# Kernel optimization log

Measured on AMD Instinct MI355X. Metric: run time of the kernel, lower is better.

The kernel has to match this reference:

```python
import jax, jax.numpy as jnp
import numpy as np

S, Q, N, T, G = 20000, 32, 200000, 30, 64
D_IN, H, D_SV, D_LANG, D_FUSE = 300, 256, 64, 64, 128

def setup_inputs() -> dict:
    key = jax.random.key(0)
    ks = jax.random.split(key, 20)
    sc = 0.05
    inp = {
        'lang_feat': jax.random.normal(ks[0], (Q, T, D_IN), jnp.float32),
        'supvox_feat': jax.random.normal(ks[1], (S, D_SV), jnp.float32),
        'supvox_coords': jax.random.uniform(ks[2], (S, 3), jnp.float32),
        'lang_len': jax.random.randint(ks[3], (Q,), 5, T + 1).astype(jnp.int32),
        'grps': jax.random.randint(ks[4], (S,), 0, G).astype(jnp.int32),
        'supervox': jax.random.randint(ks[5], (N,), 0, S).astype(jnp.int32),
        'gt': jax.random.randint(ks[6], (N, Q), 0, 2).astype(jnp.int32),
        # GRU params (torch layout: [3H, in])
        'gru_w_ih': sc * jax.random.normal(ks[7], (3 * H, D_IN), jnp.float32),
        'gru_w_hh': sc * jax.random.normal(ks[8], (3 * H, H), jnp.float32),
        'gru_b_ih': sc * jax.random.normal(ks[9], (3 * H,), jnp.float32),
        'gru_b_hh': sc * jax.random.normal(ks[10], (3 * H,), jnp.float32),
        # lang_sqz: Linear(256,64) ReLU Linear(64,64)
        'sqz_w1': sc * jax.random.normal(ks[11], (D_LANG, H), jnp.float32),
        'sqz_b1': sc * jax.random.normal(ks[12], (D_LANG,), jnp.float32),
        'sqz_w2': sc * jax.random.normal(ks[13], (D_LANG, D_LANG), jnp.float32),
        'sqz_b2': sc * jax.random.normal(ks[14], (D_LANG,), jnp.float32),
        # feat_fuse: Linear(131,128) ReLU
        'fuse_w': sc * jax.random.normal(ks[15], (D_FUSE, D_SV + 3 + D_LANG), jnp.float32),
        'fuse_b': sc * jax.random.normal(ks[16], (D_FUSE,), jnp.float32),
        # heat_map: Linear(128,2) (Dropout = identity in eval)
        'heat_w': sc * jax.random.normal(ks[17], (2, D_FUSE), jnp.float32),
        'heat_b': sc * jax.random.normal(ks[18], (2,), jnp.float32),
    }
    return inp

def _gru_last(x, lens, w_ih, w_hh, b_ih, b_hh):
    # x: [Q, T, D_IN]; returns hidden at step lens[q]-1 (pack_padded_sequence semantics)
    def step(h, xt_t):
        xt, t = xt_t  # xt: [Q, D_IN]
        gi = xt @ w_ih.T + b_ih          # [Q, 3H]
        gh = h @ w_hh.T + b_hh           # [Q, 3H]
        ir, iz, inn = jnp.split(gi, 3, -1)
        hr, hz, hn = jnp.split(gh, 3, -1)
        r = jax.nn.sigmoid(ir + hr)
        z = jax.nn.sigmoid(iz + hz)
        n = jnp.tanh(inn + r * hn)
        h_new = (1.0 - z) * n + z * h
        h = jnp.where((t < lens)[:, None], h_new, h)
        return h, None
    h0 = jnp.zeros((x.shape[0], w_hh.shape[1]), x.dtype)
    hT, _ = jax.lax.scan(step, h0, (jnp.swapaxes(x, 0, 1), jnp.arange(x.shape[1])))
    return hT  # [Q, H]

def reference(lang_feat, supvox_feat, supvox_coords, lang_len, grps, supervox, gt,
              gru_w_ih, gru_w_hh, gru_b_ih, gru_b_hh,
              sqz_w1, sqz_b1, sqz_w2, sqz_b2, fuse_w, fuse_b, heat_w, heat_b):
    # language branch
    h = _gru_last(lang_feat, lang_len, gru_w_ih, gru_w_hh, gru_b_ih, gru_b_hh)  # [Q,H]
    lang = jax.nn.relu(h @ sqz_w1.T + sqz_b1) @ sqz_w2.T + sqz_b2               # [Q,64]
    # supervoxel branch: cat(feat, coords) -> [S,67]
    sv = jnp.concatenate([supvox_feat, supvox_coords], -1)
    # feat_fuse on cat(sv, lang): split the weight to avoid materializing [S,Q,131]
    d_sv = sv.shape[-1]
    sv_proj = sv @ fuse_w[:, :d_sv].T           # [S,128]
    lang_proj = lang @ fuse_w[:, d_sv:].T       # [Q,128]
    fused = jax.nn.relu(sv_proj[:, None, :] + lang_proj[None, :, :] + fuse_b)  # [S,Q,128]
    logits = fused @ heat_w.T + heat_b          # [S,Q,2]
    obj_score = jax.nn.softmax(logits, -1)[..., 1]  # [S,Q]
    # cluster-grouped mean score (grps_ one-hot; assumes unique(grps)==arange(G))
    grp_oh = (grps[:, None] == jnp.arange(G)).astype(obj_score.dtype)  # [S,G]
    grp_sum = jnp.einsum('sq,sg->qg', obj_score, grp_oh)               # [Q,G]
    sen_grp_score = grp_sum / grp_oh.sum(0)[None, :]                   # [Q,G]
    best = jnp.argmax(sen_grp_score, -1)        # [Q]
    supvox_sen = grp_oh[:, best]                # [S,Q] binary
    obj_pts = supvox_sen[supervox].astype(jnp.int32)  # [N,Q]
    inter = (obj_pts * gt).sum(0).astype(jnp.float32)
    union = jnp.bitwise_or(obj_pts, gt).sum(0).astype(jnp.float32)
    ious = inter / (union + 1e-5)               # [Q]
    return obj_pts, ious
```

## Files before the change

### kernel.cpp

```cpp
#include <hip/hip_runtime.h>
#include <hip/hip_bf16.h>
#include <math.h>

#define S_TOT 20000
#define Q_TOT 32
#define N_TOT 200000
#define T_MAX 30
#define G_TOT 64
#define D_IN 300
#define H_DIM 256
#define D_SV 64
#define D_LANG 64
#define D_FUSE 128
#define D_CAT 67
#define FW_LD 131
#define SCHUNK 32
#define NBLK3 (S_TOT / SCHUNK)
#define SENT64 0xFFFFFFFFFFFFFFFFull
#define PCHUNK 16
#define PTILES 40

#define GI_MT 32
#define GI_NT 64
#define GI_KC 100
#define GI_NB 12
#define GI_GRID (30 * GI_NB)
#define HG_ELEMS (30 * Q_TOT * H_DIM)

#define SYNCS_N 160

__device__ __forceinline__ float sigmoidf_(float x) { return 1.0f / (1.0f + expf(-x)); }
__device__ __forceinline__ unsigned long long pack2(float a, float b) {
    return ((unsigned long long)__float_as_uint(b) << 32) | (unsigned long long)__float_as_uint(a);
}
__device__ __forceinline__ void tick_wait(int* c, int tgt) {
    __syncthreads();
    if (threadIdx.x == 0) {
        while (__hip_atomic_load(c, __ATOMIC_RELAXED, __HIP_MEMORY_SCOPE_AGENT) < tgt)
            __builtin_amdgcn_s_sleep(4);
    }
    __syncthreads();
}
__device__ __forceinline__ void tick_bump(int* c) {
    asm volatile("s_waitcnt vmcnt(0)" ::: "memory");
    if (threadIdx.x == 0)
        __hip_atomic_fetch_add(c, 1, __ATOMIC_RELAXED, __HIP_MEMORY_SCOPE_AGENT);
}

__global__ __launch_bounds__(128) void k_gi(const float* __restrict__ lang_feat,
                                            const float* __restrict__ w_ih,
                                            const float* __restrict__ b_ih,
                                            const float* __restrict__ fuse_w,
                                            const float* __restrict__ sqz_w1,
                                            const float* __restrict__ sqz_w2,
                                            const float* __restrict__ heat_w,
                                            float* __restrict__ gi,
                                            float* __restrict__ fwt,
                                            float* __restrict__ w1t,
                                            float* __restrict__ w2t,
                                            float* __restrict__ wdr,
                                            float* __restrict__ hg,
                                            int* __restrict__ syncs) {
    const int tid = threadIdx.x;
    if (blockIdx.x >= GI_GRID) {
        const int xb = blockIdx.x - GI_GRID;
        if (xb == 0) {
            for (int i = tid; i < FW_LD * D_FUSE; i += 128)
                fwt[(i % FW_LD) * D_FUSE + (i / FW_LD)] = fuse_w[i];
            for (int i = tid; i < D_LANG * H_DIM; i += 128)
                w1t[(i & 255) * D_LANG + (i >> 8)] = sqz_w1[i];
            for (int i = tid; i < D_LANG * D_LANG; i += 128)
                w2t[(i & 63) * D_LANG + (i >> 6)] = sqz_w2[i];
            if (tid < D_FUSE) wdr[tid] = heat_w[D_FUSE + tid] - heat_w[tid];
        } else {
            const int fb = xb - 1;
            const int per4 = HG_ELEMS / 4 / 8;
            float4* dst = (float4*)hg + fb * per4;
            const float4 sv = make_float4(__uint_as_float(0xFFFFFFFFu), __uint_as_float(0xFFFFFFFFu),
                                          __uint_as_float(0xFFFFFFFFu), __uint_as_float(0xFFFFFFFFu));
            for (int i = tid; i < per4; i += 128) dst[i] = sv;
            if (fb == 0) for (int i = tid; i < SYNCS_N; i += 128) syncs[i] = 0;
        }
        return;
    }
    __shared__ float x_l[GI_KC][GI_MT + 1];
    __shared__ float w_l[GI_KC][GI_NT + 1];
    const int mb = blockIdx.x / GI_NB, nb = blockIdx.x % GI_NB;
    const int m0 = mb * GI_MT, n0 = nb * GI_NT;
    const int tq4 = (tid >> 4) * 4, jq4 = (tid & 15) * 4;

    float acc[4][4];
    #pragma unroll
    for (int i = 0; i < 4; ++i)
        #pragma unroll
        for (int j = 0; j < 4; ++j) acc[i][j] = 0.f;

    for (int kc = 0; kc < 3; ++kc) {
        const int k0 = kc * GI_KC;
        for (int i = tid; i < GI_MT * GI_KC; i += 128) {
            const int r = i / GI_KC, k = i % GI_KC;
            const int row = m0 + r, q = row / T_MAX, t = row - q * T_MAX;
            x_l[k][r] = lang_feat[(q * T_MAX + t) * D_IN + k0 + k];
        }
        for (int i = tid; i < GI_NT * GI_KC; i += 128) {
            const int r = i / GI_KC, k = i % GI_KC;
            w_l[k][r] = w_ih[(n0 + r) * D_IN + k0 + k];
        }
        __syncthreads();
        #pragma unroll 2
        for (int k = 0; k < GI_KC; ++k) {
            const float x0 = x_l[k][tq4 + 0], x1 = x_l[k][tq4 + 1];
            const float x2 = x_l[k][tq4 + 2], x3 = x_l[k][tq4 + 3];
            const float v0 = w_l[k][jq4 + 0], v1 = w_l[k][jq4 + 1];
            const float v2 = w_l[k][jq4 + 2], v3 = w_l[k][jq4 + 3];
            acc[0][0] = fmaf(x0, v0, acc[0][0]); acc[0][1] = fmaf(x0, v1, acc[0][1]);
            acc[0][2] = fmaf(x0, v2, acc[0][2]); acc[0][3] = fmaf(x0, v3, acc[0][3]);
            acc[1][0] = fmaf(x1, v0, acc[1][0]); acc[1][1] = fmaf(x1, v1, acc[1][1]);
            acc[1][2] = fmaf(x1, v2, acc[1][2]); acc[1][3] = fmaf(x1, v3, acc[1][3]);
            acc[2][0] = fmaf(x2, v0, acc[2][0]); acc[2][1] = fmaf(x2, v1, acc[2][1]);
            acc[2][2] = fmaf(x2, v2, acc[2][2]); acc[2][3] = fmaf(x2, v3, acc[2][3]);
            acc[3][0] = fmaf(x3, v0, acc[3][0]); acc[3][1] = fmaf(x3, v1, acc[3][1]);
            acc[3][2] = fmaf(x3, v2, acc[3][2]); acc[3][3] = fmaf(x3, v3, acc[3][3]);
        }
        __syncthreads();
    }
    const float b0 = b_ih[n0 + jq4 + 0], b1 = b_ih[n0 + jq4 + 1];
    const float b2 = b_ih[n0 + jq4 + 2], b3 = b_ih[n0 + jq4 + 3];
    #pragma unroll
    for (int i = 0; i < 4; ++i) {
        const int row = m0 + tq4 + i;
        const int q = row / T_MAX, t = row - q * T_MAX;
        float4 v = make_float4(acc[i][0] + b0, acc[i][1] + b1, acc[i][2] + b2, acc[i][3] + b3);
        *(float4*)&gi[(q * T_MAX + t) * 768 + n0 + jq4] = v;
    }
}

__global__ __launch_bounds__(384, 1) void k_gru8(const float* __restrict__ gi,
                                                 const float* __restrict__ w_hh,
                                                 const float* __restrict__ b_hh,
                                                 const int* __restrict__ lang_len,
                                                 float* __restrict__ hg,
                                                 float* __restrict__ hbuf,
                                                 const float* __restrict__ w1t,
                                                 const float* __restrict__ b1,
                                                 const float* __restrict__ w2t,
                                                 const float* __restrict__ b2,
                                                 const float* __restrict__ fwt,
                                                 const float* __restrict__ fuse_b,
                                                 float* __restrict__ langc,
                                                 int* __restrict__ qdone) {
    __shared__ __align__(16) float wlds[96 * 256];
    __shared__ __align__(16) float hlq[4 * 68];
    __shared__ float ghl[96];
    __shared__ float gil[T_MAX * 96];

    const int tid = threadIdx.x;
    const int q = blockIdx.x >> 3, b = blockIdx.x & 7;
    int len = lang_len[q]; if (len > T_MAX) len = T_MAX; if (len < 1) len = 1;

    {
        const float4* src4 = (const float4*)w_hh;
        float4* dst4 = (float4*)wlds;
        for (int i = tid; i < 96 * 64; i += 384) {
            const int r = i >> 6, c = i & 63;
            const int grow = ((r >> 5) << 8) + (b << 5) + (r & 31);
            dst4[r * 64 + (c ^ (r & 7))] = src4[grow * 64 + c];
        }
    }
    for (int i = tid; i < len * 96; i += 384) {
        const int t = i / 96, r = i % 96;
        gil[i] = gi[(q * T_MAX + t) * 768 + ((r >> 5) << 8) + (b << 5) + (r & 31)];
    }
    __syncthreads();

    float hfin = 0.f;
    {
        float hnew = 0.f;
        if (tid < 32) {
            const float bhr = b_hh[(b << 5) + tid];
            const float bhz = b_hh[H_DIM + (b << 5) + tid];
            const float bhn = b_hh[2 * H_DIM + (b << 5) + tid];
            const float r = sigmoidf_(gil[tid] + bhr);
            const float z = sigmoidf_(gil[32 + tid] + bhz);
            const float n = tanhf(gil[64 + tid] + r * bhn);
            hnew = (1.f - z) * n;
            if (len == 1) hfin = hnew;
        }
        if (tid < 64 && len > 1) {
            const float a0 = __shfl(hnew, 2 * (tid & 15));
            const float a1 = __shfl(hnew, 2 * (tid & 15) + 1);
            if (tid < 16) {
                unsigned long long* dst = (unsigned long long*)(hg + q * H_DIM + (b << 5));
                __hip_atomic_store(dst + tid, pack2(a0, a1), __ATOMIC_RELAXED, __HIP_MEMORY_SCOPE_AGENT);
            }
        }
    }

    const int row = tid >> 2, ql = tid & 3;
    const float bh = b_hh[((row >> 5) << 8) + (b << 5) + (row & 31)];
    const int rx = row & 7;
    const float4* wrow4 = (const float4*)wlds + row * 64;
    const int cbase = ql << 4;

    for (int t = 1; t < len; ++t) {
        if (tid < 128) {
            const unsigned long long* src =
                (const unsigned long long*)(hg + (size_t)(t - 1) * (Q_TOT * H_DIM) + q * H_DIM);
            unsigned long long v;
            while ((v = __hip_atomic_load(src + tid, __ATOMIC_RELAXED,
                                          __HIP_MEMORY_SCOPE_AGENT)) == SENT64)
                __builtin_amdgcn_s_sleep(1);
            const int k = 2 * tid;
            const int o = (k >> 6) * 68 + (k & 63);
            hlq[o]     = __uint_as_float((unsigned)(v & 0xffffffffu));
            hlq[o + 1] = __uint_as_float((unsigned)(v >> 32));
        }
        __syncthreads();
        float hold = 0.f;
        if (tid < 32) { const int k = (b << 5) + tid; hold = hlq[(k >> 6) * 68 + (k & 63)]; }
        const float4* h4 = (const float4*)(hlq + ql * 68);
        float ax = 0.f, ay = 0.f, az = 0.f, aw = 0.f;
        #pragma unroll
        for (int i = 0; i < 16; ++i) {
            const float4 wv = wrow4[(cbase + i) ^ rx];
            const float4 hv = h4[i];
            ax = fmaf(wv.x, hv.x, ax);
            ay = fmaf(wv.y, hv.y, ay);
            az = fmaf(wv.z, hv.z, az);
            aw = fmaf(wv.w, hv.w, aw);
        }
        float s = (ax + ay) + (az + aw);
        s += __shfl_xor(s, 1);
        s += __shfl_xor(s, 2);
        if (ql == 0) ghl[row] = s + bh;
        __syncthreads();
        float hnew = 0.f;
        if (tid < 32) {
            const float* gt_ = gil + t * 96;
            const float r = sigmoidf_(gt_[tid] + ghl[tid]);
            const float z = sigmoidf_(gt_[32 + tid] + ghl[32 + tid]);
            const float n = tanhf(gt_[64 + tid] + r * ghl[64 + tid]);
            hnew = (1.f - z) * n + z * hold;
            if (t == len - 1) hfin = hnew;
        }
        if (tid < 64 && t < len - 1) {
            const float a0 = __shfl(hnew, 2 * (tid & 15));
            const float a1 = __shfl(hnew, 2 * (tid & 15) + 1);
            if (tid < 16) {
                unsigned long long* dst =
                    (unsigned long long*)(hg + (size_t)t * (Q_TOT * H_DIM) + q * H_DIM + (b << 5));
                __hip_atomic_store(dst + tid, pack2(a0, a1), __ATOMIC_RELAXED, __HIP_MEMORY_SCOPE_AGENT);
            }
        }
    }

    if (tid < 32)
        __hip_atomic_store(&hbuf[q * H_DIM + (b << 5) + tid], hfin,
                           __ATOMIC_RELAXED, __HIP_MEMORY_SCOPE_AGENT);
    asm volatile("s_waitcnt vmcnt(0)" ::: "memory");
    __syncthreads();
    if (tid == 0)
        __hip_atomic_fetch_add(&qdone[q], 1, __ATOMIC_RELAXED, __HIP_MEMORY_SCOPE_AGENT);
    if (b != 0) return;

    if (tid == 0) {
        while (__hip_atomic_load(&qdone[q], __ATOMIC_RELAXED, __HIP_MEMORY_SCOPE_AGENT) < 8)
            __builtin_amdgcn_s_sleep(2);
    }
    __syncthreads();
    float* hql = gil;
    float* t1l = gil + 256;
    float* lgl = gil + 320;
    if (tid < H_DIM)
        hql[tid] = __hip_atomic_load(&hbuf[q * H_DIM + tid], __ATOMIC_RELAXED, __HIP_MEMORY_SCOPE_AGENT);
    __syncthreads();
    if (tid < 256) {
        const int c = tid >> 2, qq = tid & 3;
        float a = 0.f;
        #pragma unroll 8
        for (int j = 0; j < 64; ++j) {
            const int k = (qq << 6) + j;
            a = fmaf(w1t[k * D_LANG + c], hql[k], a);
        }
        a += __shfl_xor(a, 1);
        a += __shfl_xor(a, 2);
        if (qq == 0) t1l[c] = fmaxf(a + b1[c], 0.f);
    }
    __syncthreads();
    if (tid < 256) {
        const int c = tid >> 2, qq = tid & 3;
        float a = 0.f;
        #pragma unroll
        for (int j = 0; j < 16; ++j) {
            const int k = (qq << 4) + j;
            a = fmaf(w2t[k * D_LANG + c], t1l[k], a);
        }
        a += __shfl_xor(a, 1);
        a += __shfl_xor(a, 2);
        if (qq == 0) lgl[c] = a + b2[c];
    }
    __syncthreads();
    if (tid < 256) {
        const int d = tid >> 1, hh = tid & 1;
        float a = 0.f;
        #pragma unroll 8
        for (int j = 0; j < 32; ++j) {
            const int k = (hh << 5) + j;
            a = fmaf(fwt[(D_CAT + k) * D_FUSE + d], lgl[k], a);
        }
        a += __shfl_xor(a, 1);
        if (hh == 0) langc[q * D_FUSE + d] = a + fuse_b[d];
    }
}

__global__ __launch_bounds__(256, 3) void k_tail(const float* __restrict__ feat,
                                                 const float* __restrict__ coords,
                                                 const int* __restrict__ grps,
                                                 const float* __restrict__ langc,
                                                 const float* __restrict__ fwt,
                                                 const float* __restrict__ wdr_g,
                                                 const float* __restrict__ heat_b,
                                                 float* __restrict__ grp_part,
                                                 int* __restrict__ cnt_part,
                                                 float* __restrict__ grp2,
                                                 int* __restrict__ cnt2,
                                                 int* __restrict__ best,
                                                 int* __restrict__ smask,
                                                 const int* __restrict__ supervox,
                                                 const int* __restrict__ gt,
                                                 float* __restrict__ out,
                                                 int* __restrict__ syncs) {
    int* interG   = syncs;
    int* unionG   = syncs + 32;
    int* t_out    = syncs + 64;
    int* gtick    = syncs + 65;
    int* qtick    = syncs + 98;
    int* t_fuse   = syncs + 130;
    int* t_smask  = syncs + 131;
    const int tid = threadIdx.x;
    const int bid = blockIdx.x;

    __shared__ __align__(16) float svin[SCHUNK][68];
    __shared__ __align__(16) float svp[SCHUNK][132];
    __shared__ float score[SCHUNK][Q_TOT];
    __shared__ int grps_l[SCHUNK];
    __shared__ float ps[4][G_TOT];
    __shared__ int   pc[4][G_TOT];
    __shared__ float sc[G_TOT];
    __shared__ int bl[Q_TOT];
    __shared__ int bi_s[Q_TOT], bu_s[Q_TOT];
    __shared__ int islast;

    {
        const int s0 = bid * SCHUNK;
        const int dsl = tid & 7, q = tid >> 3;
        float lc[16], wdr[16];
        #pragma unroll
        for (int i = 0; i < 16; ++i) {
            const int d = dsl * 16 + i;
            lc[i]  = langc[q * D_FUSE + d];
            wdr[i] = wdr_g[d];
        }
        const float hbd = heat_b[1] - heat_b[0];

        for (int i = tid; i < SCHUNK * D_SV; i += 256) {
            const int r = i >> 6, c = i & 63;
            svin[r][c] = feat[(s0 + r) * D_SV + c];
        }
        if (tid < SCHUNK * 3) { const int r = tid / 3, c = tid % 3; svin[r][D_SV + c] = coords[(s0 + r) * 3 + c]; }
        if (tid < SCHUNK) grps_l[tid] = grps[s0 + tid];
        __syncthreads();

        {
            const int d = tid & 127, sl0 = tid >> 7;
            float acc[16];
            #pragma unroll
            for (int i = 0; i < 16; ++i) acc[i] = 0.f;
            for (int k4 = 0; k4 < 16; ++k4) {
                const float w0 = fwt[(4 * k4 + 0) * D_FUSE + d];
                const float w1 = fwt[(4 * k4 + 1) * D_FUSE + d];
                const float w2 = fwt[(4 * k4 + 2) * D_FUSE + d];
                const float w3 = fwt[(4 * k4 + 3) * D_FUSE + d];
                #pragma unroll
                for (int i = 0; i < 16; ++i) {
                    const float4 xv = *(const float4*)&svin[sl0 + 2 * i][4 * k4];
                    acc[i] = fmaf(xv.x, w0, fmaf(xv.y, w1, fmaf(xv.z, w2, fmaf(xv.w, w3, acc[i]))));
                }
            }
            for (int k = 64; k < D_CAT; ++k) {
                const float wv = fwt[k * D_FUSE + d];
                #pragma unroll
                for (int i = 0; i < 16; ++i)
                    acc[i] = fmaf(svin[sl0 + 2 * i][k], wv, acc[i]);
            }
            #pragma unroll
            for (int i = 0; i < 16; ++i) svp[sl0 + 2 * i][d] = acc[i];
        }
        __syncthreads();

        for (int sl = 0; sl < SCHUNK; ++sl) {
            const float4* sv4 = (const float4*)(&svp[sl][dsl * 16]);
            float part = 0.f;
            #pragma unroll
            for (int j = 0; j < 4; ++j) {
                const float4 v = sv4[j];
                part = fmaf(fmaxf(v.x + lc[4*j+0], 0.f), wdr[4*j+0], part);
                part = fmaf(fmaxf(v.y + lc[4*j+1], 0.f), wdr[4*j+1], part);
                part = fmaf(fmaxf(v.z + lc[4*j+2], 0.f), wdr[4*j+2], part);
                part = fmaf(fmaxf(v.w + lc[4*j+3], 0.f), wdr[4*j+3], part);
            }
            part += __shfl_xor(part, 1);
            part += __shfl_xor(part, 2);
            part += __shfl_xor(part, 4);
            if (dsl == 0) score[sl][q] = sigmoidf_(part + hbd);
        }
        __syncthreads();

        for (int i = 0; i < 8; ++i) {
            const int cell = tid + 256 * i;
            const int qq = cell >> 6, g = cell & 63;
            float sum = 0.f;
            #pragma unroll
            for (int sl = 0; sl < SCHUNK; ++sl)
                sum += (grps_l[sl] == g) ? score[sl][qq] : 0.f;
            __hip_atomic_store(&grp_part[bid * (Q_TOT * G_TOT) + cell], sum,
                               __ATOMIC_RELAXED, __HIP_MEMORY_SCOPE_AGENT);
            if (cell < G_TOT) {
                int c = 0;
                #pragma unroll
                for (int sl = 0; sl < SCHUNK; ++sl) c += (grps_l[sl] == g);
                __hip_atomic_store(&cnt_part[bid * G_TOT + g], c,
                                   __ATOMIC_RELAXED, __HIP_MEMORY_SCOPE_AGENT);
            }
        }
        tick_bump(t_fuse);
    }
    tick_wait(t_fuse, NBLK3);

    if (bid < Q_TOT * PCHUNK) {
        const int q = bid & 31, c = bid >> 5;
        const int bq = tid >> 6, g = tid & 63;
        const int b0 = c * PTILES;
        int b1 = b0 + PTILES; if (b1 > NBLK3) b1 = NBLK3;
        float acc = 0.f; int cacc = 0;
        for (int b = b0 + bq; b < b1; b += 4) {
            acc  += grp_part[b * (Q_TOT * G_TOT) + q * G_TOT + g];
            cacc += cnt_part[b * G_TOT + g];
        }
        ps[bq][g] = acc; pc[bq][g] = cacc;
        __syncthreads();
        if (tid < G_TOT) {
            const float s = ((ps[0][tid] + ps[1][tid]) + ps[2][tid]) + ps[3][tid];
            const int  cc = ((pc[0][tid] + pc[1][tid]) + pc[2][tid]) + pc[3][tid];
            __hip_atomic_store(&grp2[(c * Q_TOT + q) * G_TOT + tid], s,
                               __ATOMIC_RELAXED, __HIP_MEMORY_SCOPE_AGENT);
            __hip_atomic_store(&cnt2[(c * Q_TOT + q) * G_TOT + tid], cc,
                               __ATOMIC_RELAXED, __HIP_MEMORY_SCOPE_AGENT);
        }
        __shared__ int myturn;
        asm volatile("s_waitcnt vmcnt(0)" ::: "memory");
        if (tid == 0) {
            const int old = __hip_atomic_fetch_add(&qtick[q], 1, __ATOMIC_RELAXED, __HIP_MEMORY_SCOPE_AGENT);
            myturn = (old == PCHUNK - 1) ? 1 : 0;
        }
        __syncthreads();
        if (myturn) {
            if (tid < G_TOT) {
                float s = 0.f; int cc = 0;
                #pragma unroll
                for (int c2 = 0; c2 < PCHUNK; ++c2) {
                    s  += grp2[(c2 * Q_TOT + q) * G_TOT + tid];
                    cc += cnt2[(c2 * Q_TOT + q) * G_TOT + tid];
                }
                sc[tid] = s / (float)cc;
            }
            __syncthreads();
            if (tid == 0) {
                float bv = sc[0]; int bi = 0;
                for (int g2 = 1; g2 < G_TOT; ++g2) if (sc[g2] > bv) { bv = sc[g2]; bi = g2; }
                __hip_atomic_store(&best[q], bi, __ATOMIC_RELAXED, __HIP_MEMORY_SCOPE_AGENT);
                asm volatile("s_waitcnt vmcnt(0)" ::: "memory");
                __hip_atomic_fetch_add(gtick, 1, __ATOMIC_RELAXED, __HIP_MEMORY_SCOPE_AGENT);
            }
        }
    }
    tick_wait(gtick, Q_TOT);

    if (tid < Q_TOT) bl[tid] = best[tid];
    __syncthreads();
    if (tid < 32) {
        const int s = bid * 32 + tid;
        const int gg = grps[s];
        int m = 0;
        #pragma unroll
        for (int qq = 0; qq < Q_TOT; ++qq) m |= (bl[qq] == gg) ? (1 << qq) : 0;
        __hip_atomic_store(&smask[s], m, __ATOMIC_RELAXED, __HIP_MEMORY_SCOPE_AGENT);
    }
    tick_bump(t_smask);
    tick_wait(t_smask, NBLK3);

    {
        const int gidx = bid * 256 + tid;
        const int q4 = (gidx & 7) * 4;
        const int nstride = (NBLK3 * 256) >> 3;
        int a0 = 0, a1 = 0, a2 = 0, a3 = 0;
        int u0 = 0, u1 = 0, u2 = 0, u3 = 0;
        for (int n = gidx >> 3; n < N_TOT; n += nstride) {
            const int m = smask[supervox[n]];
            const int4 g4 = *(const int4*)&gt[n * Q_TOT + q4];
            const int o0 = (m >> (q4 + 0)) & 1;
            const int o1 = (m >> (q4 + 1)) & 1;
            const int o2 = (m >> (q4 + 2)) & 1;
            const int o3 = (m >> (q4 + 3)) & 1;
            *(float4*)&out[n * Q_TOT + q4] =
                make_float4((float)o0, (float)o1, (float)o2, (float)o3);
            a0 += o0 & g4.x; u0 += o0 | g4.x;
            a1 += o1 & g4.y; u1 += o1 | g4.y;
            a2 += o2 & g4.z; u2 += o2 | g4.z;
            a3 += o3 & g4.w; u3 += o3 | g4.w;
        }
        if (tid < Q_TOT) { bi_s[tid] = 0; bu_s[tid] = 0; }
        __syncthreads();
        atomicAdd(&bi_s[q4 + 0], a0); atomicAdd(&bu_s[q4 + 0], u0);
        atomicAdd(&bi_s[q4 + 1], a1); atomicAdd(&bu_s[q4 + 1], u1);
        atomicAdd(&bi_s[q4 + 2], a2); atomicAdd(&bu_s[q4 + 2], u2);
        atomicAdd(&bi_s[q4 + 3], a3); atomicAdd(&bu_s[q4 + 3], u3);
        __syncthreads();
        if (tid < Q_TOT) { atomicAdd(&interG[tid], bi_s[tid]); atomicAdd(&unionG[tid], bu_s[tid]); }
        asm volatile("s_waitcnt vmcnt(0)" ::: "memory");
        if (tid == 0) {
            const int old = __hip_atomic_fetch_add(t_out, 1, __ATOMIC_RELAXED, __HIP_MEMORY_SCOPE_AGENT);
            islast = (old == NBLK3 - 1) ? 1 : 0;
        }
        __syncthreads();
        if (islast && tid < Q_TOT) {
            const int iv = __hip_atomic_load(&interG[tid], __ATOMIC_RELAXED, __HIP_MEMORY_SCOPE_AGENT);
            const int uv = __hip_atomic_load(&unionG[tid], __ATOMIC_RELAXED, __HIP_MEMORY_SCOPE_AGENT);
            out[(size_t)N_TOT * Q_TOT + tid] = (float)iv / ((float)uv + 1e-5f);
        }
    }
}

extern "C" void kernel_launch(void* const* d_in, const int* in_sizes, int n_in,
                              void* d_out, int out_size, void* d_ws, size_t ws_size,
                              hipStream_t stream) {
    const float* lang_feat = (const float*)d_in[0];
    const float* feat      = (const float*)d_in[1];
    const float* coords    = (const float*)d_in[2];
    const int*   lang_len  = (const int*)d_in[3];
    const int*   grps      = (const int*)d_in[4];
    const int*   supervox  = (const int*)d_in[5];
    const int*   gt        = (const int*)d_in[6];
    const float* w_ih      = (const float*)d_in[7];
    const float* w_hh      = (const float*)d_in[8];
    const float* b_ih      = (const float*)d_in[9];
    const float* b_hh      = (const float*)d_in[10];
    const float* sqz_w1    = (const float*)d_in[11];
    const float* sqz_b1    = (const float*)d_in[12];
    const float* sqz_w2    = (const float*)d_in[13];
    const float* sqz_b2    = (const float*)d_in[14];
    const float* fuse_w    = (const float*)d_in[15];
    const float* fuse_b    = (const float*)d_in[16];
    const float* heat_w    = (const float*)d_in[17];
    const float* heat_b    = (const float*)d_in[18];
    float* out = (float*)d_out;

    float* gi       = (float*)d_ws;
    float* hbuf     = gi + 737280;
    float* langc    = hbuf + 8192;
    float* grp_part = langc + 4096;
    int*   cnt_part = (int*)(grp_part + NBLK3 * 2048);
    int*   best     = cnt_part + NBLK3 * 64;
    int*   smask    = best + 32;
    int*   syncs    = smask + S_TOT;
    float* hg       = (float*)(syncs + SYNCS_N);
    float* fwt      = hg + HG_ELEMS;
    float* w1t      = fwt + FW_LD * D_FUSE;
    float* w2t      = w1t + H_DIM * D_LANG;
    float* wdr      = w2t + D_LANG * D_LANG;
    float* grp2     = wdr + 128;
    int*   cnt2     = (int*)(grp2 + PCHUNK * Q_TOT * G_TOT);

    k_gi   <<<GI_GRID + 9, 128, 0, stream>>>(lang_feat, w_ih, b_ih, fuse_w, sqz_w1, sqz_w2, heat_w,
                                             gi, fwt, w1t, w2t, wdr, hg, syncs);
    k_gru8 <<<Q_TOT * 8, 384, 0, stream>>>(gi, w_hh, b_hh, lang_len, hg, hbuf,
                                           w1t, sqz_b1, w2t, sqz_b2, fwt, fuse_b, langc,
                                           syncs + 66);
    k_tail <<<NBLK3, 256, 0, stream>>>(feat, coords, grps, langc, fwt, wdr, heat_b,
                                       grp_part, cnt_part, grp2, cnt2, best, smask,
                                       supervox, gt, out, syncs);
}
```

Before: 234.2 us.

## Replace global grid barriers with per-chunk counters and flag broadcast, drop smask pass

Replaces the all-block barrier after the fuse phase with per-chunk counters, so each partial-reduce block waits only for the PTILES blocks it reads. The group-reduce barrier becomes a set of flags, spread over eight cache lines and written by the last finisher, which cuts contention from polling. The global smask array and its grid-wide barrier go away: each block builds a 64-entry group-to-query mask in shared memory and indexes it through grps[supervox[n]]. The cost is one extra indirect load per point in the output loop. Each block also still spins on a flag.

```diff
diff --git a/kernel.cpp b/kernel.cpp
--- a/kernel.cpp
+++ b/kernel.cpp
@@ -27,24 +27,11 @@
 #define GI_GRID (30 * GI_NB)
 #define HG_ELEMS (30 * Q_TOT * H_DIM)
 
-#define SYNCS_N 160
+#define SYNCS_N 1024
 
 __device__ __forceinline__ float sigmoidf_(float x) { return 1.0f / (1.0f + expf(-x)); }
 __device__ __forceinline__ unsigned long long pack2(float a, float b) {
     return ((unsigned long long)__float_as_uint(b) << 32) | (unsigned long long)__float_as_uint(a);
-}
-__device__ __forceinline__ void tick_wait(int* c, int tgt) {
-    __syncthreads();
-    if (threadIdx.x == 0) {
-        while (__hip_atomic_load(c, __ATOMIC_RELAXED, __HIP_MEMORY_SCOPE_AGENT) < tgt)
-            __builtin_amdgcn_s_sleep(4);
-    }
-    __syncthreads();
-}
-__device__ __forceinline__ void tick_bump(int* c) {
-    asm volatile("s_waitcnt vmcnt(0)" ::: "memory");
-    if (threadIdx.x == 0)
-        __hip_atomic_fetch_add(c, 1, __ATOMIC_RELAXED, __HIP_MEMORY_SCOPE_AGENT);
 }
 
 __global__ __launch_bounds__(128) void k_gi(const float* __restrict__ lang_feat,
@@ -325,18 +312,15 @@
                                                  float* __restrict__ grp2,
                                                  int* __restrict__ cnt2,
                                                  int* __restrict__ best,
-                                                 int* __restrict__ smask,
                                                  const int* __restrict__ supervox,
                                                  const int* __restrict__ gt,
                                                  float* __restrict__ out,
                                                  int* __restrict__ syncs) {
-    int* interG   = syncs;
-    int* unionG   = syncs + 32;
-    int* t_out    = syncs + 64;
-    int* gtick    = syncs + 65;
-    int* qtick    = syncs + 98;
-    int* t_fuse   = syncs + 130;
-    int* t_smask  = syncs + 131;
+    int* interG = syncs;
+    int* unionG = syncs + 32;
+    int* t_out  = syncs + 64;
+    int* gtick  = syncs + 65;
+    int* qtick  = syncs + 98;
     const int tid = threadIdx.x;
     const int bid = blockIdx.x;
 
@@ -348,6 +332,7 @@
     __shared__ int   pc[4][G_TOT];
     __shared__ float sc[G_TOT];
     __shared__ int bl[Q_TOT];
+    __shared__ int gm[G_TOT];
     __shared__ int bi_s[Q_TOT], bu_s[Q_TOT];
     __shared__ int islast;
 
@@ -433,15 +418,25 @@
                                    __ATOMIC_RELAXED, __HIP_MEMORY_SCOPE_AGENT);
             }
         }
-        tick_bump(t_fuse);
-    }
-    tick_wait(t_fuse, NBLK3);
+        asm volatile("s_waitcnt vmcnt(0)" ::: "memory");
+        __syncthreads();
+        if (tid == 0)
+            __hip_atomic_fetch_add(&syncs[160 + 32 * (bid / PTILES)], 1,
+                                   __ATOMIC_RELAXED, __HIP_MEMORY_SCOPE_AGENT);
+    }
 
     if (bid < Q_TOT * PCHUNK) {
         const int q = bid & 31, c = bid >> 5;
-        const int bq = tid >> 6, g = tid & 63;
         const int b0 = c * PTILES;
         int b1 = b0 + PTILES; if (b1 > NBLK3) b1 = NBLK3;
+        if (tid == 0) {
+            int* tc = &syncs[160 + 32 * c];
+            const int tgt = b1 - b0;
+            while (__hip_atomic_load(tc, __ATOMIC_RELAXED, __HIP_MEMORY_SCOPE_AGENT) < tgt)
+                __builtin_amdgcn_s_sleep(4);
+        }
+        __syncthreads();
+        const int bq = tid >> 6, g = tid & 63;
         float acc = 0.f; int cacc = 0;
         for (int b = b0 + bq; b < b1; b += 4) {
             acc  += grp_part[b * (Q_TOT * G_TOT) + q * G_TOT + g];
@@ -480,24 +475,33 @@
                 for (int g2 = 1; g2 < G_TOT; ++g2) if (sc[g2] > bv) { bv = sc[g2]; bi = g2; }
                 __hip_atomic_store(&best[q], bi, __ATOMIC_RELAXED, __HIP_MEMORY_SCOPE_AGENT);
                 asm volatile("s_waitcnt vmcnt(0)" ::: "memory");
-                __hip_atomic_fetch_add(gtick, 1, __ATOMIC_RELAXED, __HIP_MEMORY_SCOPE_AGENT);
-            }
-        }
-    }
-    tick_wait(gtick, Q_TOT);
+                const int old = __hip_atomic_fetch_add(gtick, 1, __ATOMIC_RELAXED, __HIP_MEMORY_SCOPE_AGENT);
+                if (old == Q_TOT - 1) {
+                    #pragma unroll
+                    for (int f = 0; f < 8; ++f)
+                        __hip_atomic_store(&syncs[672 + 32 * f], 1,
+                                           __ATOMIC_RELAXED, __HIP_MEMORY_SCOPE_AGENT);
+                }
+            }
+        }
+    }
+
+    if (tid == 0) {
+        int* fl = &syncs[672 + 32 * (bid & 7)];
+        while (__hip_atomic_load(fl, __ATOMIC_RELAXED, __HIP_MEMORY_SCOPE_AGENT) == 0)
+            __builtin_amdgcn_s_sleep(16);
+    }
+    __syncthreads();
 
     if (tid < Q_TOT) bl[tid] = best[tid];
     __syncthreads();
-    if (tid < 32) {
-        const int s = bid * 32 + tid;
-        const int gg = grps[s];
+    if (tid < G_TOT) {
         int m = 0;
         #pragma unroll
-        for (int qq = 0; qq < Q_TOT; ++qq) m |= (bl[qq] == gg) ? (1 << qq) : 0;
-        __hip_atomic_store(&smask[s], m, __ATOMIC_RELAXED, __HIP_MEMORY_SCOPE_AGENT);
-    }
-    tick_bump(t_smask);
-    tick_wait(t_smask, NBLK3);
+        for (int qq = 0; qq < Q_TOT; ++qq) m |= (bl[qq] == tid) ? (1 << qq) : 0;
+        gm[tid] = m;
+    }
+    __syncthreads();
 
     {
         const int gidx = bid * 256 + tid;
@@ -506,7 +510,7 @@
         int a0 = 0, a1 = 0, a2 = 0, a3 = 0;
         int u0 = 0, u1 = 0, u2 = 0, u3 = 0;
         for (int n = gidx >> 3; n < N_TOT; n += nstride) {
-            const int m = smask[supervox[n]];
+            const int m = gm[grps[supervox[n]]];
             const int4 g4 = *(const int4*)&gt[n * Q_TOT + q4];
             const int o0 = (m >> (q4 + 0)) & 1;
             const int o1 = (m >> (q4 + 1)) & 1;
@@ -571,8 +575,7 @@
     float* grp_part = langc + 4096;
     int*   cnt_part = (int*)(grp_part + NBLK3 * 2048);
     int*   best     = cnt_part + NBLK3 * 64;
-    int*   smask    = best + 32;
-    int*   syncs    = smask + S_TOT;
+    int*   syncs    = best + 32;
     float* hg       = (float*)(syncs + SYNCS_N);
     float* fwt      = hg + HG_ELEMS;
     float* w1t      = fwt + FW_LD * D_FUSE;
@@ -587,6 +590,6 @@
                                            w1t, sqz_b1, w2t, sqz_b2, fwt, fuse_b, langc,
                                            syncs + 66);
     k_tail <<<NBLK3, 256, 0, stream>>>(feat, coords, grps, langc, fwt, wdr, heat_b,
-                                       grp_part, cnt_part, grp2, cnt2, best, smask,
+                                       grp_part, cnt_part, grp2, cnt2, best,
                                        supervox, gt, out, syncs);
 }
```

Measured after the change: 202.7 us (median of 2 runs). 13.4% less time.
